# Performance work log

Hardware: AMD Instinct MI355X
Metric: run time of the kernel (lower is better)

Reference implementation:

```python
import jax, jax.numpy as jnp
import numpy as np

N_NODES = 200000
N_EDGES = 3200000
F_IN = 128
CH = 32
N_GRAPHS = 1024
N_LABELS = 17


def setup_inputs() -> dict:
    key = jax.random.key(0)
    ks = jax.random.split(key, 16)
    x = jax.random.normal(ks[0], (N_NODES, F_IN), dtype=jnp.float32)
    a_row = jax.random.randint(ks[1], (N_EDGES,), 0, N_NODES, dtype=jnp.int64)
    a_col = jax.random.randint(ks[2], (N_EDGES,), 0, N_NODES, dtype=jnp.int64)
    a_val = jax.random.uniform(ks[3], (N_EDGES,), dtype=jnp.float32)
    seg = jnp.sort(jax.random.randint(ks[4], (N_NODES,), 0, N_GRAPHS, dtype=jnp.int64))
    def glorot(k, fan_in, fan_out):
        lim = np.sqrt(6.0 / (fan_in + fan_out)).astype(np.float32)
        return jax.random.uniform(k, (fan_in, fan_out), dtype=jnp.float32, minval=-lim, maxval=lim)
    params = {
        'W1_1': glorot(ks[5], F_IN, CH), 'W2_1': glorot(ks[6], F_IN, CH), 'b_1': jnp.zeros((CH,), jnp.float32),
        'W1_2': glorot(ks[7], CH, CH),   'W2_2': glorot(ks[8], CH, CH),   'b_2': jnp.zeros((CH,), jnp.float32),
        'W1_3': glorot(ks[9], CH, CH),   'W2_3': glorot(ks[10], CH, CH),  'b_3': jnp.zeros((CH,), jnp.float32),
        'Wd': glorot(ks[11], CH, N_LABELS), 'bd': jnp.zeros((N_LABELS,), jnp.float32),
    }
    return dict(x=x, a_row=a_row, a_col=a_col, a_val=a_val, seg=seg, **params)


def _gcs_conv(x, a_row, a_col, a_val, W1, W2, b):
    # A @ X via gather(col) -> weight -> scatter-add(row)
    msgs = a_val[:, None] * x[a_col]            # [E, F]
    agg = jax.ops.segment_sum(msgs, a_row, num_segments=N_NODES)  # [N, F]
    return jax.nn.relu(agg @ W1 + x @ W2 + b)


def reference(x, a_row, a_col, a_val, seg,
              W1_1, W2_1, b_1, W1_2, W2_2, b_2, W1_3, W2_3, b_3, Wd, bd):
    h = _gcs_conv(x, a_row, a_col, a_val, W1_1, W2_1, b_1)
    h = _gcs_conv(h, a_row, a_col, a_val, W1_2, W2_2, b_2)
    h = _gcs_conv(h, a_row, a_col, a_val, W1_3, W2_3, b_3)
    # GlobalAvgPool over batch index i: segment mean per graph
    sums = jax.ops.segment_sum(h, seg, num_segments=N_GRAPHS)          # [G, CH]
    cnts = jax.ops.segment_sum(jnp.ones((N_NODES,), h.dtype), seg, num_segments=N_GRAPHS)
    pooled = sums / jnp.maximum(cnts, 1.0)[:, None]
    return jax.nn.softmax(pooled @ Wd + bd, axis=-1)
```

## Files before the change

### kernel.cpp

```cpp
#include <hip/hip_runtime.h>
#include <cstdint>

#define N_NODES 200000
#define N_EDGES 3200000
#define F_IN 128
#define CH 32
#define N_GRAPHS 1024
#define N_LABELS 17

#define BROWS 512
#define NBUCK ((N_NODES + BROWS - 1) / BROWS)
#define CAP 10240
#define EPB 8192

typedef unsigned int uint32;
typedef unsigned short u16;

#define TSCALE 16.f

__device__ __forceinline__ u16 f2bf(float f) {
  unsigned int u = __float_as_uint(f);
  u = (u + 0x7FFFu + ((u >> 16) & 1u)) >> 16;
  return (u16)u;
}
__device__ __forceinline__ float bf2f(u16 h) {
  return __uint_as_float(((unsigned int)h) << 16);
}
__device__ __forceinline__ signed char f2q8(float f) {
  float qf = fmaxf(-127.f, fminf(127.f, rintf(f * TSCALE)));
  return (signed char)(int)qf;
}


__global__ __launch_bounds__(256) void k_passA(const int* __restrict__ arow,
                                               const int* __restrict__ acol,
                                               const float* __restrict__ aval,
                                               int* __restrict__ bucketCur,
                                               unsigned long long* __restrict__ records) {
  __shared__ int cnt[NBUCK];
  __shared__ int base[NBUCK];
  int t = threadIdx.x;
  for (int i = t; i < NBUCK; i += 256) cnt[i] = 0;
  __syncthreads();
  int e0 = blockIdx.x * EPB;
  int e1 = e0 + EPB; if (e1 > N_EDGES) e1 = N_EDGES;
  for (int e = e0 + t; e < e1; e += 256) atomicAdd(&cnt[arow[e] >> 9], 1);
  __syncthreads();
  for (int i = t; i < NBUCK; i += 256) {
    int n = cnt[i];
    base[i] = n ? atomicAdd(&bucketCur[i], n) : 0;
    cnt[i] = 0;
  }
  __syncthreads();
  for (int e = e0 + t; e < e1; e += 256) {
    int r = arow[e];
    int b = r >> 9;
    int p = atomicAdd(&cnt[b], 1) + base[b];
    if (p < CAP) {
      unsigned int hi = ((unsigned int)(r & 511) << 18) | (unsigned int)acol[e];
      unsigned long long rec = ((unsigned long long)hi << 32) |
                               (unsigned int)__float_as_int(aval[e]);
      records[(size_t)b * CAP + p] = rec;
    }
  }
}


__global__ __launch_bounds__(512) void k_passB(const int* __restrict__ bucketCur,
                                               const unsigned long long* __restrict__ records,
                                               int2* __restrict__ rowinfo,
                                               uint32* __restrict__ edges) {
  __shared__ int cnt[BROWS];
  __shared__ int sc[BROWS];
  __shared__ int cur[BROWS];
  int b = blockIdx.x;
  int t = threadIdx.x;
  int nrec = bucketCur[b]; if (nrec > CAP) nrec = CAP;
  const unsigned long long* rp = records + (size_t)b * CAP;
  cnt[t] = 0;
  __syncthreads();
  for (int i = t; i < nrec; i += 512) {
    unsigned int hi = (unsigned int)(rp[i] >> 32);
    atomicAdd(&cnt[hi >> 18], 1);
  }
  __syncthreads();
  sc[t] = cnt[t];
  __syncthreads();
  for (int d = 1; d < BROWS; d <<= 1) {
    int v = (t >= d) ? sc[t - d] : 0;
    __syncthreads();
    sc[t] += v;
    __syncthreads();
  }
  int pre = sc[t] - cnt[t];
  cur[t] = pre;
  int r = b * BROWS + t;
  if (r < N_NODES) rowinfo[r] = make_int2(b * CAP + pre, cnt[t]);
  __syncthreads();
  for (int i = t; i < nrec; i += 512) {
    unsigned long long rec = rp[i];
    unsigned int hi = (unsigned int)(rec >> 32);
    int rl = hi >> 18;
    unsigned int col = hi & 0x3FFFFu;
    float val = __int_as_float((int)(unsigned int)rec);
    int q = (int)fmaf(val, 16383.f, 0.5f);
    q = q < 0 ? 0 : (q > 16383 ? 16383 : q);
    int p = atomicAdd(&cur[rl], 1);
    edges[(size_t)b * CAP + p] = (col << 14) | (unsigned int)q;
  }
}


__global__ __launch_bounds__(256) void k_dense1(const float* __restrict__ x,
                                                const float* __restrict__ W1,
                                                const float* __restrict__ W2,
                                                signed char* __restrict__ tout,
                                                u16* __restrict__ sout) {
  int i = blockIdx.x * blockDim.x + threadIdx.x;
  if (i >= N_NODES) return;
  const float* xr = x + (size_t)i * F_IN;
  float acc1[CH], acc2[CH];
#pragma unroll
  for (int c = 0; c < CH; c++) { acc1[c] = 0.f; acc2[c] = 0.f; }
#pragma unroll 8
  for (int k = 0; k < F_IN; k += 4) {
    float4 xv = *(const float4*)(xr + k);
    float xk[4] = {xv.x, xv.y, xv.z, xv.w};
#pragma unroll
    for (int kk = 0; kk < 4; kk++) {
      float xval = xk[kk];
      const float* w1r = W1 + (size_t)(k + kk) * CH;
      const float* w2r = W2 + (size_t)(k + kk) * CH;
#pragma unroll
      for (int c = 0; c < CH; c++) {
        acc1[c] = fmaf(xval, w1r[c], acc1[c]);
        acc2[c] = fmaf(xval, w2r[c], acc2[c]);
      }
    }
  }
  uint32* tp = (uint32*)(tout + (size_t)i * CH);
#pragma unroll
  for (int c = 0; c < CH; c += 4) {
    uint32 p = ((uint32)(unsigned char)f2q8(acc1[c])) |
               ((uint32)(unsigned char)f2q8(acc1[c + 1]) << 8) |
               ((uint32)(unsigned char)f2q8(acc1[c + 2]) << 16) |
               ((uint32)(unsigned char)f2q8(acc1[c + 3]) << 24);
    tp[c >> 2] = p;
  }
  uint32* sp = (uint32*)(sout + (size_t)i * CH);
#pragma unroll
  for (int c = 0; c < CH; c += 2) {
    sp[c >> 1] = (uint32)f2bf(acc2[c]) | ((uint32)f2bf(acc2[c + 1]) << 16);
  }
}


template <int MODE>
__global__ __launch_bounds__(256) void k_gcs(const int2* __restrict__ rowinfo,
                                             const uint32* __restrict__ edges,
                                             const signed char* __restrict__ tin,
                                             u16* __restrict__ sio,
                                             const float* __restrict__ bias,
                                             const float* __restrict__ W1n,
                                             const float* __restrict__ W2n,
                                             signed char* __restrict__ tout,
                                             float* __restrict__ hout) {
  int gid = blockIdx.x * blockDim.x + threadIdx.x;
  int node = gid >> 5;
  int c = gid & 31;
  if (node >= N_NODES) return;
  int2 ri = rowinfo[node];
  const uint32* ep = edges + ri.x;
  int n = ri.y;
  float s = bf2f(sio[((size_t)node << 5) + c]);
  float a0 = 0.f, a1 = 0.f, a2 = 0.f, a3 = 0.f;
  for (int e = 0; e < n; e += 16) {
    int el = e + (c & 15);
    uint32 me = ep[el < n ? el : n - 1];
    uint32 d[16];
#pragma unroll
    for (int j = 0; j < 16; j++) d[j] = __shfl(me, j, 32) ;
    int g[16];
#pragma unroll
    for (int j = 0; j < 16; j++) {
      g[j] = (int)tin[((size_t)(d[j] >> 14) << 5) + c];
    }
#pragma unroll
    for (int j = 0; j < 16; j++) {
      float v = (e + j < n) ? (float)(d[j] & 0x3FFFu) : 0.f;
      if ((j & 3) == 0) a0 = fmaf(v, (float)g[j], a0);
      else if ((j & 3) == 1) a1 = fmaf(v, (float)g[j], a1);
      else if ((j & 3) == 2) a2 = fmaf(v, (float)g[j], a2);
      else a3 = fmaf(v, (float)g[j], a3);
    }
  }
  float acc = ((a0 + a1) + (a2 + a3)) * (1.f / (16383.f * TSCALE));
  float h = fmaxf(acc + s + bias[c], 0.f);
  if (MODE == 1) {
    hout[((size_t)node << 5) + c] = h;
  } else {
    float m1 = 0.f, m2 = 0.f;
#pragma unroll
    for (int k = 0; k < CH; k++) {
      float hk = __shfl(h, k, 32);
      m1 = fmaf(hk, W1n[k * CH + c], m1);
      m2 = fmaf(hk, W2n[k * CH + c], m2);
    }
    tout[((size_t)node << 5) + c] = f2q8(m1);
    sio[((size_t)node << 5) + c] = f2bf(m2);
  }
}


__global__ void k_head(const float* __restrict__ h, const int* __restrict__ seg,
                       const float* __restrict__ Wd, const float* __restrict__ bd,
                       float* __restrict__ out) {
  int g = blockIdx.x;
  int t = threadIdx.x;
  __shared__ float red[64];
  __shared__ float pooled[CH];
  __shared__ float logits[N_LABELS];
  int lo, hi;
  {
    int l = 0, r = N_NODES;
    while (l < r) { int m = (l + r) >> 1; if (seg[m] < g) l = m + 1; else r = m; }
    lo = l;
  }
  {
    int l = 0, r = N_NODES;
    while (l < r) { int m = (l + r) >> 1; if (seg[m] < g + 1) l = m + 1; else r = m; }
    hi = l;
  }
  float acc = 0.f;
  int c = t & 31, half = t >> 5;
  for (int i = lo + half; i < hi; i += 2) acc += h[(size_t)i * CH + c];
  red[t] = acc;
  __syncthreads();
  if (t < CH) {
    float cnt = (float)((hi - lo) > 0 ? (hi - lo) : 1);
    pooled[t] = (red[t] + red[t + 32]) / cnt;
  }
  __syncthreads();
  if (t < N_LABELS) {
    float a = bd[t];
#pragma unroll
    for (int k = 0; k < CH; k++) a = fmaf(pooled[k], Wd[k * N_LABELS + t], a);
    logits[t] = a;
  }
  __syncthreads();
  if (t == 0) {
    float mx = logits[0];
    for (int j = 1; j < N_LABELS; j++) mx = fmaxf(mx, logits[j]);
    float ssum = 0.f;
    float e[N_LABELS];
    for (int j = 0; j < N_LABELS; j++) { e[j] = expf(logits[j] - mx); ssum += e[j]; }
    float inv = 1.f / ssum;
    for (int j = 0; j < N_LABELS; j++) out[(size_t)g * N_LABELS + j] = e[j] * inv;
  }
}


extern "C" void kernel_launch(void* const* d_in, const int* in_sizes, int n_in,
                              void* d_out, int out_size, void* d_ws, size_t ws_size,
                              hipStream_t stream) {
  const float* x    = (const float*)d_in[0];
  const int*   arow = (const int*)d_in[1];
  const int*   acol = (const int*)d_in[2];
  const float* aval = (const float*)d_in[3];
  const int*   seg  = (const int*)d_in[4];
  const float* W1_1 = (const float*)d_in[5];
  const float* W2_1 = (const float*)d_in[6];
  const float* b_1  = (const float*)d_in[7];
  const float* W1_2 = (const float*)d_in[8];
  const float* W2_2 = (const float*)d_in[9];
  const float* b_2  = (const float*)d_in[10];
  const float* W1_3 = (const float*)d_in[11];
  const float* W2_3 = (const float*)d_in[12];
  const float* b_3  = (const float*)d_in[13];
  const float* Wd   = (const float*)d_in[14];
  const float* bd   = (const float*)d_in[15];
  float* out = (float*)d_out;

  char* w = (char*)d_ws;
  signed char* tA = (signed char*)w; w += (size_t)N_NODES * CH;
  signed char* tB = (signed char*)w; w += (size_t)N_NODES * CH;
  u16* sS = (u16*)w;                 w += (size_t)N_NODES * CH * 2;
  float* hbuf = (float*)w;           w += (size_t)N_NODES * CH * 4;
  uint32* edges = (uint32*)w;        w += (size_t)NBUCK * CAP * 4;
  int2* rowinfo = (int2*)w;          w += (size_t)N_NODES * 8;
  int* bucketCur = (int*)w;          w += 4096;
  unsigned long long* records = (unsigned long long*)d_ws;

  hipMemsetAsync(bucketCur, 0, (size_t)NBUCK * 4, stream);
  k_passA<<<(N_EDGES + EPB - 1) / EPB, 256, 0, stream>>>(arow, acol, aval, bucketCur, records);
  k_passB<<<NBUCK, 512, 0, stream>>>(bucketCur, records, rowinfo, edges);

  k_dense1<<<(N_NODES + 255) / 256, 256, 0, stream>>>(x, W1_1, W2_1, tA, sS);

  const int GCS_GRID = (N_NODES * 32 + 255) / 256;
  k_gcs<0><<<GCS_GRID, 256, 0, stream>>>(rowinfo, edges, tA, sS, b_1, W1_2, W2_2, tB, nullptr);
  k_gcs<0><<<GCS_GRID, 256, 0, stream>>>(rowinfo, edges, tB, sS, b_2, W1_3, W2_3, tA, nullptr);
  k_gcs<1><<<GCS_GRID, 256, 0, stream>>>(rowinfo, edges, tA, sS, b_3, nullptr, nullptr, nullptr, hbuf);

  k_head<<<N_GRAPHS, 64, 0, stream>>>(hbuf, seg, Wd, bd, out);
}
```

Measured before the change: 411.3 us.

## Transpose x into bf16 feature-major layout before first dense layer

Adds a kernel that reads x in coalesced float4 rows, converts each value to bf16, and writes it through an LDS tile into a feature-major buffer (pairs of features per uint32). The first dense kernel then reads this transposed buffer so that consecutive threads load consecutive addresses, instead of each thread striding through its own 512-byte row. This aims to fix uncoalesced global loads in k_dense1 and halve the bytes it reads. In exchange it adds an extra kernel launch, an extra write and read of the transposed buffer, and bf16 rounding of the input features.

```diff
diff --git a/kernel.cpp b/kernel.cpp
--- a/kernel.cpp
+++ b/kernel.cpp
@@ -17,6 +17,7 @@
 typedef unsigned short u16;
 
 #define TSCALE 16.f
+#define TSTRIDE 130
 
 __device__ __forceinline__ u16 f2bf(float f) {
   unsigned int u = __float_as_uint(f);
@@ -111,34 +112,66 @@
 }
 
 
-__global__ __launch_bounds__(256) void k_dense1(const float* __restrict__ x,
+__global__ __launch_bounds__(256) void k_xpose(const float* __restrict__ x,
+                                               uint32* __restrict__ xT) {
+  __shared__ u16 tile[256 * TSTRIDE];
+  int t = threadIdx.x;
+  size_t wgNode = (size_t)blockIdx.x * 256;
+  const float4* x4 = (const float4*)x;
+#pragma unroll
+  for (int j = 0; j < 32; j++) {
+    int idx = t + 256 * j;
+    int row = idx >> 5;
+    int sub = idx & 31;
+    if (wgNode + (size_t)row < N_NODES) {
+      float4 v = x4[wgNode * 32 + idx];
+      uint32 lo = (uint32)f2bf(v.x) | ((uint32)f2bf(v.y) << 16);
+      uint32 hi = (uint32)f2bf(v.z) | ((uint32)f2bf(v.w) << 16);
+      uint32* dst = (uint32*)&tile[row * TSTRIDE + sub * 4];
+      dst[0] = lo;
+      dst[1] = hi;
+    }
+  }
+  __syncthreads();
+  size_t node = wgNode + t;
+  if (node >= N_NODES) return;
+#pragma unroll
+  for (int kp = 0; kp < 64; kp++) {
+    uint32 v = *(const uint32*)&tile[t * TSTRIDE + kp * 2];
+    xT[(size_t)kp * N_NODES + node] = v;
+  }
+}
+
+
+__global__ __launch_bounds__(256) void k_dense1(const uint32* __restrict__ xT,
                                                 const float* __restrict__ W1,
                                                 const float* __restrict__ W2,
                                                 signed char* __restrict__ tout,
                                                 u16* __restrict__ sout) {
-  int i = blockIdx.x * blockDim.x + threadIdx.x;
-  if (i >= N_NODES) return;
-  const float* xr = x + (size_t)i * F_IN;
+  int node = blockIdx.x * blockDim.x + threadIdx.x;
+  if (node >= N_NODES) return;
   float acc1[CH], acc2[CH];
 #pragma unroll
   for (int c = 0; c < CH; c++) { acc1[c] = 0.f; acc2[c] = 0.f; }
 #pragma unroll 8
-  for (int k = 0; k < F_IN; k += 4) {
-    float4 xv = *(const float4*)(xr + k);
-    float xk[4] = {xv.x, xv.y, xv.z, xv.w};
-#pragma unroll
-    for (int kk = 0; kk < 4; kk++) {
-      float xval = xk[kk];
-      const float* w1r = W1 + (size_t)(k + kk) * CH;
-      const float* w2r = W2 + (size_t)(k + kk) * CH;
-#pragma unroll
-      for (int c = 0; c < CH; c++) {
-        acc1[c] = fmaf(xval, w1r[c], acc1[c]);
-        acc2[c] = fmaf(xval, w2r[c], acc2[c]);
-      }
-    }
-  }
-  uint32* tp = (uint32*)(tout + (size_t)i * CH);
+  for (int kp = 0; kp < 64; kp++) {
+    uint32 wv = xT[(size_t)kp * N_NODES + node];
+    float xlo = bf2f((u16)(wv & 0xffffu));
+    float xhi = bf2f((u16)(wv >> 16));
+    const float* w1r = W1 + (size_t)(2 * kp) * CH;
+    const float* w2r = W2 + (size_t)(2 * kp) * CH;
+#pragma unroll
+    for (int c = 0; c < CH; c++) {
+      acc1[c] = fmaf(xlo, w1r[c], acc1[c]);
+      acc2[c] = fmaf(xlo, w2r[c], acc2[c]);
+    }
+#pragma unroll
+    for (int c = 0; c < CH; c++) {
+      acc1[c] = fmaf(xhi, w1r[CH + c], acc1[c]);
+      acc2[c] = fmaf(xhi, w2r[CH + c], acc2[c]);
+    }
+  }
+  uint32* tp = (uint32*)(tout + (size_t)node * CH);
 #pragma unroll
   for (int c = 0; c < CH; c += 4) {
     uint32 p = ((uint32)(unsigned char)f2q8(acc1[c])) |
@@ -147,7 +180,7 @@
                ((uint32)(unsigned char)f2q8(acc1[c + 3]) << 24);
     tp[c >> 2] = p;
   }
-  uint32* sp = (uint32*)(sout + (size_t)i * CH);
+  uint32* sp = (uint32*)(sout + (size_t)node * CH);
 #pragma unroll
   for (int c = 0; c < CH; c += 2) {
     sp[c >> 1] = (uint32)f2bf(acc2[c]) | ((uint32)f2bf(acc2[c + 1]) << 16);
@@ -179,7 +212,7 @@
     uint32 me = ep[el < n ? el : n - 1];
     uint32 d[16];
 #pragma unroll
-    for (int j = 0; j < 16; j++) d[j] = __shfl(me, j, 32) ;
+    for (int j = 0; j < 16; j++) d[j] = __shfl(me, j, 32);
     int g[16];
 #pragma unroll
     for (int j = 0; j < 16; j++) {
@@ -289,13 +322,16 @@
   uint32* edges = (uint32*)w;        w += (size_t)NBUCK * CAP * 4;
   int2* rowinfo = (int2*)w;          w += (size_t)N_NODES * 8;
   int* bucketCur = (int*)w;          w += 4096;
+  uint32* xT = (uint32*)w;           w += (size_t)64 * N_NODES * 4;
   unsigned long long* records = (unsigned long long*)d_ws;
 
   hipMemsetAsync(bucketCur, 0, (size_t)NBUCK * 4, stream);
   k_passA<<<(N_EDGES + EPB - 1) / EPB, 256, 0, stream>>>(arow, acol, aval, bucketCur, records);
   k_passB<<<NBUCK, 512, 0, stream>>>(bucketCur, records, rowinfo, edges);
 
-  k_dense1<<<(N_NODES + 255) / 256, 256, 0, stream>>>(x, W1_1, W2_1, tA, sS);
+  k_xpose<<<(N_NODES + 255) / 256, 256, 0, stream>>>(x, xT);
+
+  k_dense1<<<(N_NODES + 255) / 256, 256, 0, stream>>>(xT, W1_1, W2_1, tA, sS);
 
   const int GCS_GRID = (N_NODES * 32 + 255) / 256;
   k_gcs<0><<<GCS_GRID, 256, 0, stream>>>(rowinfo, edges, tA, sS, b_1, W1_2, W2_2, tB, nullptr);
```

Result: slower. 463.2 us (+12.6%).
